# Kernel tuning notes

Measured on AMD Instinct MI355X. Metric: run time of the kernel, lower is better.

## Reference

```python
import jax, jax.numpy as jnp
import numpy as np

N_DST = 50000
NUM_HEAD = 2
LN_EPS = 1e-5


def setup_inputs() -> dict:
    key = jax.random.key(0)
    ks = jax.random.split(key, 12)
    n_dst, n_src, E = 50000, 200000, 250000
    dim_node, dim_edge, dim_time, dim_out = 128, 64, 64, 128
    d_q = dim_node + dim_time            # w_q input dim
    d_k = dim_node + dim_edge + dim_time  # w_k / w_v input dim
    d_o = dim_node + dim_out              # w_out input dim
    f32 = jnp.float32
    return {
        "h": jax.random.normal(ks[0], (n_dst + n_src, dim_node), f32),
        "dt": jax.random.uniform(ks[1], (E,), f32) * 100.0,
        "ef": jax.random.normal(ks[2], (E, dim_edge), f32),
        # TimeEncode: cos(t * w + b), classic TGAT init w = 1/10^linspace(0,9)
        "time_w": (1.0 / 10.0 ** jnp.linspace(0.0, 9.0, dim_time)).astype(f32),
        "time_b": jnp.zeros((dim_time,), f32),
        "wq_w": (jax.random.normal(ks[3], (d_q, dim_out), f32) / np.sqrt(d_q)),
        "wq_b": jnp.zeros((dim_out,), f32),
        "wk_w": (jax.random.normal(ks[4], (d_k, dim_out), f32) / np.sqrt(d_k)),
        "wk_b": jnp.zeros((dim_out,), f32),
        "wv_w": (jax.random.normal(ks[5], (d_k, dim_out), f32) / np.sqrt(d_k)),
        "wv_b": jnp.zeros((dim_out,), f32),
        "wo_w": (jax.random.normal(ks[6], (d_o, dim_out), f32) / np.sqrt(d_o)),
        "wo_b": jnp.zeros((dim_out,), f32),
        "ln_g": jnp.ones((dim_out,), f32),
        "ln_b": jnp.zeros((dim_out,), f32),
        "nbr_idx": jax.random.randint(ks[7], (E,), 0, n_src),
        "edge_dst": jax.random.randint(ks[8], (E,), 0, n_dst),
    }


def reference(h, dt, ef, time_w, time_b, wq_w, wq_b, wk_w, wk_b, wv_w, wv_b,
              wo_w, wo_b, ln_g, ln_b, nbr_idx, edge_dst):
    n_dst = N_DST
    H = NUM_HEAD
    h_dst = h[:n_dst]                       # [n_dst, D]
    h_src = h[n_dst:]                       # [n_src, D]

    # time encoding: cos(t * w + b)
    time_feat = jnp.cos(dt[:, None] * time_w + time_b)          # [E, Dt]
    zero_time = jnp.broadcast_to(jnp.cos(time_b), (n_dst, time_b.shape[0]))

    Q_in = jnp.concatenate([h_dst, zero_time], axis=1)           # [n_dst, D+Dt]
    K_in = jnp.concatenate([h_src[nbr_idx], ef, time_feat], axis=1)  # [E, D+De+Dt]

    Q = (Q_in @ wq_w + wq_b)[edge_dst]      # [E, dim_out] gathered per edge
    K = K_in @ wk_w + wk_b                  # [E, dim_out]
    V = K_in @ wv_w + wv_b                  # [E, dim_out]

    E_ = Q.shape[0]
    Qh = Q.reshape(E_, H, -1)
    Kh = K.reshape(E_, H, -1)
    Vh = V.reshape(E_, H, -1)

    att_raw = jax.nn.leaky_relu(jnp.sum(Qh * Kh, axis=2), 0.2)   # [E, H]

    # edge_softmax: segment softmax over incoming edges of each dst node
    m = jax.ops.segment_max(att_raw, edge_dst, num_segments=n_dst)
    m = jnp.where(jnp.isfinite(m), m, 0.0)  # guard empty segments
    ex = jnp.exp(att_raw - m[edge_dst])
    den = jax.ops.segment_sum(ex, edge_dst, num_segments=n_dst)
    att = ex / den[edge_dst]                # [E, H]

    Vw = (Vh * att[..., None]).reshape(E_, -1)                   # [E, dim_out]
    agg = jax.ops.segment_sum(Vw, edge_dst, num_segments=n_dst)  # [n_dst, dim_out]

    pre = jax.nn.relu(jnp.concatenate([agg, h_dst], axis=1) @ wo_w + wo_b)
    mu = jnp.mean(pre, axis=-1, keepdims=True)
    var = jnp.var(pre, axis=-1, keepdims=True)
    return (pre - mu) / jnp.sqrt(var + LN_EPS) * ln_g + ln_b
```

## Files before the change

### kernel.cpp

```cpp
#include <hip/hip_runtime.h>
#include <hip/hip_bf16.h>
#include <math.h>


using bf16 = __hip_bfloat16;
typedef __attribute__((ext_vector_type(8))) short short8;
typedef __attribute__((ext_vector_type(4))) float f32x4;

static __device__ __forceinline__ unsigned short bf16_bits(float x) {
    bf16 h = __float2bfloat16(x);
    unsigned short b;
    __builtin_memcpy(&b, &h, 2);
    return b;
}
static __device__ __forceinline__ unsigned pk2(float x, float y) {
    return (unsigned)bf16_bits(x) | ((unsigned)bf16_bits(y) << 16);
}
static __device__ __forceinline__ float bflo(unsigned u) {
    return __uint_as_float(u << 16);
}
static __device__ __forceinline__ float bfhi(unsigned u) {
    return __uint_as_float(u & 0xffff0000u);
}
union frag_u { short8 s; unsigned u[4]; };

__global__ void k_prep(float* qbias, const float* __restrict__ wq_w,
                       const float* __restrict__ wq_b, const float* __restrict__ time_b) {
    int c = threadIdx.x;
    if (c < 128) {
        float s = wq_b[c];
        for (int j = 0; j < 64; ++j)
            s += cosf(time_b[j]) * wq_w[(128 + j) * 128 + c];
        qbias[c] = s;
    }
}

__global__ void k_pack(unsigned short* wkT, unsigned short* wvT, unsigned short* woT,
                       unsigned short* wqhT, unsigned short* wqlT,
                       const float* __restrict__ wk_w, const float* __restrict__ wv_w,
                       const float* __restrict__ wo_w, const float* __restrict__ wq_w) {
    int idx = blockIdx.x * blockDim.x + threadIdx.x;
    if (idx < 32768) {
        int n = idx >> 8, k = idx & 255;
        wkT[idx] = bf16_bits(wk_w[(size_t)k * 128 + n]);
        wvT[idx] = bf16_bits(wv_w[(size_t)k * 128 + n]);
        woT[idx] = bf16_bits(wo_w[(size_t)k * 128 + n]);
        if (idx < 16384) {
            int n2 = idx >> 7, k2 = idx & 127;
            float v = wq_w[(size_t)k2 * 128 + n2];
            unsigned short hb = bf16_bits(v);
            wqhT[idx] = hb;
            wqlT[idx] = bf16_bits(v - __uint_as_float((unsigned)hb << 16));
        }
    }
}

__global__ void k_count(const int* __restrict__ edst, int* cnt, int E) {
    int e = blockIdx.x * 256 + threadIdx.x;
    if (e < E) atomicAdd(&cnt[edst[e]], 1);
}

__global__ void k_scan1(const int* __restrict__ cnt, int* rs, int* bsum, int n) {
    __shared__ int s[256];
    int t = threadIdx.x;
    int i = blockIdx.x * 256 + t;
    int v = (i < n) ? cnt[i] : 0;
    s[t] = v;
    __syncthreads();
    for (int off = 1; off < 256; off <<= 1) {
        int x = (t >= off) ? s[t - off] : 0;
        __syncthreads();
        s[t] += x;
        __syncthreads();
    }
    if (i < n) rs[i] = s[t] - v;
    if (t == 255) bsum[blockIdx.x] = s[255];
}

__global__ void k_scan2(int* bsum, int nblk) {
    __shared__ int s[256];
    int t = threadIdx.x;
    int v = (t < nblk) ? bsum[t] : 0;
    s[t] = v;
    __syncthreads();
    for (int off = 1; off < 256; off <<= 1) {
        int x = (t >= off) ? s[t - off] : 0;
        __syncthreads();
        s[t] += x;
        __syncthreads();
    }
    if (t < nblk) bsum[t] = s[t] - v;
}

__global__ void k_scan3(int* rs, const int* __restrict__ bsum, int n) {
    int i = blockIdx.x * 256 + threadIdx.x;
    if (i < n) rs[i] += bsum[blockIdx.x];
}

__global__ void k_scatter(const int* __restrict__ edst, const int* __restrict__ rs,
                          int* fill, int* epos, int E) {
    int e = blockIdx.x * 256 + threadIdx.x;
    if (e < E) {
        int d = edst[e];
        epos[e] = rs[d] + atomicAdd(&fill[d], 1);
    }
}

__global__ __launch_bounds__(256) void k_q(
    float* __restrict__ Q, const float* __restrict__ h,
    const unsigned short* __restrict__ wqhT, const unsigned short* __restrict__ wqlT,
    const float* __restrict__ qbias, int ndst)
{
    __shared__ unsigned short Bs[16384];
    int tid = threadIdx.x;
    int lane = tid & 63, l15 = lane & 15, lk = lane >> 4;
    int r0 = blockIdx.x * 64 + (tid >> 6) * 16;
    int ra = r0 + l15;
    int rc = (ra < ndst) ? ra : (ndst - 1);
    const float* hrow = h + (size_t)rc * 128;

    float4 hx[4][2];
    #pragma unroll
    for (int kk = 0; kk < 4; ++kk) {
        int c0 = kk * 32 + lk * 8;
        hx[kk][0] = *reinterpret_cast<const float4*>(hrow + c0);
        hx[kk][1] = *reinterpret_cast<const float4*>(hrow + c0 + 4);
    }

    #pragma unroll
    for (int it = 0; it < 8; ++it) {
        int i = it * 256 + tid;
        int row = i >> 4, c = i & 15;
        uint4 v = *reinterpret_cast<const uint4*>(wqhT + (size_t)row * 128 + c * 8);
        *reinterpret_cast<uint4*>(Bs + row * 128 + ((c ^ (row & 15)) << 3)) = v;
    }

    frag_u ah[4], al[4];
    #pragma unroll
    for (int kk = 0; kk < 4; ++kk) {
        float xs[8] = {hx[kk][0].x, hx[kk][0].y, hx[kk][0].z, hx[kk][0].w,
                       hx[kk][1].x, hx[kk][1].y, hx[kk][1].z, hx[kk][1].w};
        unsigned short hb[8];
        float lo[8];
        #pragma unroll
        for (int t = 0; t < 8; ++t) {
            hb[t] = bf16_bits(xs[t]);
            lo[t] = xs[t] - __uint_as_float((unsigned)hb[t] << 16);
        }
        #pragma unroll
        for (int t = 0; t < 4; ++t)
            ah[kk].u[t] = (unsigned)hb[2*t] | ((unsigned)hb[2*t+1] << 16);
        al[kk].u[0] = pk2(lo[0], lo[1]); al[kk].u[1] = pk2(lo[2], lo[3]);
        al[kk].u[2] = pk2(lo[4], lo[5]); al[kk].u[3] = pk2(lo[6], lo[7]);
    }

    f32x4 ck[8];
    #pragma unroll
    for (int nt = 0; nt < 8; ++nt) ck[nt] = (f32x4){0.f, 0.f, 0.f, 0.f};

    __syncthreads();
    #pragma unroll
    for (int kk2 = 0; kk2 < 4; ++kk2) {
        int co = ((kk2 * 4 + lk) ^ l15) << 3;
        #pragma unroll
        for (int nt = 0; nt < 8; ++nt) {
            short8 b = *reinterpret_cast<const short8*>(Bs + (nt * 16 + l15) * 128 + co);
            ck[nt] = __builtin_amdgcn_mfma_f32_16x16x32_bf16(ah[kk2].s, b, ck[nt], 0, 0, 0);
            ck[nt] = __builtin_amdgcn_mfma_f32_16x16x32_bf16(al[kk2].s, b, ck[nt], 0, 0, 0);
        }
    }
    __syncthreads();
    #pragma unroll
    for (int it = 0; it < 8; ++it) {
        int i = it * 256 + tid;
        int row = i >> 4, c = i & 15;
        uint4 v = *reinterpret_cast<const uint4*>(wqlT + (size_t)row * 128 + c * 8);
        *reinterpret_cast<uint4*>(Bs + row * 128 + ((c ^ (row & 15)) << 3)) = v;
    }
    __syncthreads();
    #pragma unroll
    for (int kk2 = 0; kk2 < 4; ++kk2) {
        int co = ((kk2 * 4 + lk) ^ l15) << 3;
        #pragma unroll
        for (int nt = 0; nt < 8; ++nt) {
            short8 b = *reinterpret_cast<const short8*>(Bs + (nt * 16 + l15) * 128 + co);
            ck[nt] = __builtin_amdgcn_mfma_f32_16x16x32_bf16(ah[kk2].s, b, ck[nt], 0, 0, 0);
        }
    }

    #pragma unroll
    for (int nt = 0; nt < 8; ++nt) {
        int col = nt * 16 + l15;
        float qb = qbias[col];
        #pragma unroll
        for (int j = 0; j < 4; ++j) {
            int row = r0 + lk * 4 + j;
            if (row < ndst) Q[(size_t)row * 128 + col] = ck[nt][j] + qb;
        }
    }
}

__global__ __launch_bounds__(256) void k_kvA(
    const float* __restrict__ h, const int* __restrict__ nbr, const int* __restrict__ edst,
    const float* __restrict__ dt, const float* __restrict__ ef,
    const float* __restrict__ time_w, const float* __restrict__ time_b,
    const unsigned short* __restrict__ wkT, const unsigned short* __restrict__ wvT,
    const float* __restrict__ wk_b, const float* __restrict__ Q,
    const int* __restrict__ epos,
    unsigned short* __restrict__ Vbuf, float2* __restrict__ att2, int ndst, int E)
{
    __shared__ unsigned short Bs[16384];
    int tid  = threadIdx.x;
    int lane = tid & 63;
    int l15  = lane & 15;
    int lk   = lane >> 4;
    int e0   = blockIdx.x * 64 + (tid >> 6) * 16;

    int  ea = e0 + l15;
    bool va = ea < E;
    int  na = va ? nbr[ea] : 0;
    float da = va ? dt[ea] : 0.f;
    const float* hrow = h + (size_t)(ndst + na) * 128;
    const float* erow = ef + (size_t)ea * 64;

    int dstr[4], pe[4];
    bool evv[4];
    #pragma unroll
    for (int j = 0; j < 4; ++j) {
        int ed = e0 + lk * 4 + j;
        evv[j]  = ed < E;
        dstr[j] = evv[j] ? edst[ed] : 0;
        pe[j]   = evv[j] ? epos[ed] : 0;
    }

    float4 hx[4][2], ex_[2][2];
    const float4 z4 = make_float4(0.f, 0.f, 0.f, 0.f);
    #pragma unroll
    for (int kk = 0; kk < 4; ++kk) {
        int c0 = kk * 32 + lk * 8;
        hx[kk][0] = va ? *reinterpret_cast<const float4*>(hrow + c0)     : z4;
        hx[kk][1] = va ? *reinterpret_cast<const float4*>(hrow + c0 + 4) : z4;
    }
    #pragma unroll
    for (int t = 0; t < 2; ++t) {
        int c = (4 + t) * 32 + lk * 8 - 128;
        ex_[t][0] = va ? *reinterpret_cast<const float4*>(erow + c)     : z4;
        ex_[t][1] = va ? *reinterpret_cast<const float4*>(erow + c + 4) : z4;
    }

    float qg[8][4];
    #pragma unroll
    for (int nt = 0; nt < 8; ++nt) {
        int gc = nt * 16 + l15;
        #pragma unroll
        for (int j = 0; j < 4; ++j)
            qg[nt][j] = Q[(size_t)dstr[j] * 128 + gc];
    }

    #pragma unroll
    for (int it = 0; it < 8; ++it) {
        int i = it * 256 + tid;
        int row = i >> 4, c = i & 15;
        uint4 v = *reinterpret_cast<const uint4*>(wkT + (size_t)row * 256 + c * 8);
        *reinterpret_cast<uint4*>(Bs + row * 128 + ((c ^ (row & 15)) << 3)) = v;
    }

    float tf[16];
    {
        int j0 = lk * 8;
        #pragma unroll
        for (int t = 0; t < 8; ++t) tf[t]     = __cosf(fmaf(da, time_w[j0 + t],      time_b[j0 + t]));
        #pragma unroll
        for (int t = 0; t < 8; ++t) tf[8 + t] = __cosf(fmaf(da, time_w[j0 + 32 + t], time_b[j0 + 32 + t]));
    }

    frag_u a[8];
    #pragma unroll
    for (int kk = 0; kk < 4; ++kk) {
        a[kk].u[0] = pk2(hx[kk][0].x, hx[kk][0].y); a[kk].u[1] = pk2(hx[kk][0].z, hx[kk][0].w);
        a[kk].u[2] = pk2(hx[kk][1].x, hx[kk][1].y); a[kk].u[3] = pk2(hx[kk][1].z, hx[kk][1].w);
    }
    #pragma unroll
    for (int t = 0; t < 2; ++t) {
        a[4+t].u[0] = pk2(ex_[t][0].x, ex_[t][0].y); a[4+t].u[1] = pk2(ex_[t][0].z, ex_[t][0].w);
        a[4+t].u[2] = pk2(ex_[t][1].x, ex_[t][1].y); a[4+t].u[3] = pk2(ex_[t][1].z, ex_[t][1].w);
    }
    a[6].u[0] = pk2(tf[0], tf[1]);  a[6].u[1] = pk2(tf[2], tf[3]);
    a[6].u[2] = pk2(tf[4], tf[5]);  a[6].u[3] = pk2(tf[6], tf[7]);
    a[7].u[0] = pk2(tf[8], tf[9]);  a[7].u[1] = pk2(tf[10], tf[11]);
    a[7].u[2] = pk2(tf[12], tf[13]); a[7].u[3] = pk2(tf[14], tf[15]);

    f32x4 ck[8];
    #pragma unroll
    for (int nt = 0; nt < 8; ++nt) ck[nt] = (f32x4){0.f, 0.f, 0.f, 0.f};

    __syncthreads();
    #pragma unroll
    for (int kk2 = 0; kk2 < 4; ++kk2) {
        int co = ((kk2 * 4 + lk) ^ l15) << 3;
        #pragma unroll
        for (int nt = 0; nt < 8; ++nt) {
            short8 b = *reinterpret_cast<const short8*>(Bs + (nt * 16 + l15) * 128 + co);
            ck[nt] = __builtin_amdgcn_mfma_f32_16x16x32_bf16(a[kk2].s, b, ck[nt], 0, 0, 0);
        }
    }
    __syncthreads();
    #pragma unroll
    for (int it = 0; it < 8; ++it) {
        int i = it * 256 + tid;
        int row = i >> 4, c = i & 15;
        uint4 v = *reinterpret_cast<const uint4*>(wkT + (size_t)row * 256 + 128 + c * 8);
        *reinterpret_cast<uint4*>(Bs + row * 128 + ((c ^ (row & 15)) << 3)) = v;
    }
    __syncthreads();
    #pragma unroll
    for (int kk2 = 0; kk2 < 4; ++kk2) {
        int co = ((kk2 * 4 + lk) ^ l15) << 3;
        #pragma unroll
        for (int nt = 0; nt < 8; ++nt) {
            short8 b = *reinterpret_cast<const short8*>(Bs + (nt * 16 + l15) * 128 + co);
            ck[nt] = __builtin_amdgcn_mfma_f32_16x16x32_bf16(a[4 + kk2].s, b, ck[nt], 0, 0, 0);
        }
    }
    __syncthreads();
    #pragma unroll
    for (int it = 0; it < 8; ++it) {
        int i = it * 256 + tid;
        int row = i >> 4, c = i & 15;
        uint4 v = *reinterpret_cast<const uint4*>(wvT + (size_t)row * 256 + c * 8);
        *reinterpret_cast<uint4*>(Bs + row * 128 + ((c ^ (row & 15)) << 3)) = v;
    }

    float p0[4], p1[4];
    #pragma unroll
    for (int j = 0; j < 4; ++j) { p0[j] = 0.f; p1[j] = 0.f; }
    #pragma unroll
    for (int nt = 0; nt < 8; ++nt) {
        float kb = wk_b[nt * 16 + l15];
        #pragma unroll
        for (int j = 0; j < 4; ++j) {
            float t = (ck[nt][j] + kb) * qg[nt][j];
            if (nt < 4) p0[j] += t; else p1[j] += t;
        }
    }
    #pragma unroll
    for (int m = 1; m <= 8; m <<= 1)
        #pragma unroll
        for (int j = 0; j < 4; ++j) {
            p0[j] += __shfl_xor(p0[j], m, 64);
            p1[j] += __shfl_xor(p1[j], m, 64);
        }
    if (l15 == 0) {
        #pragma unroll
        for (int j = 0; j < 4; ++j)
            if (evv[j]) {
                float r0 = p0[j]; r0 = (r0 >= 0.f) ? r0 : 0.2f * r0;
                float r1 = p1[j]; r1 = (r1 >= 0.f) ? r1 : 0.2f * r1;
                att2[pe[j]] = make_float2(r0, r1);
            }
    }

    f32x4 cv[8];
    #pragma unroll
    for (int nt = 0; nt < 8; ++nt) cv[nt] = (f32x4){0.f, 0.f, 0.f, 0.f};
    __syncthreads();
    #pragma unroll
    for (int kk2 = 0; kk2 < 4; ++kk2) {
        int co = ((kk2 * 4 + lk) ^ l15) << 3;
        #pragma unroll
        for (int nt = 0; nt < 8; ++nt) {
            short8 b = *reinterpret_cast<const short8*>(Bs + (nt * 16 + l15) * 128 + co);
            cv[nt] = __builtin_amdgcn_mfma_f32_16x16x32_bf16(a[kk2].s, b, cv[nt], 0, 0, 0);
        }
    }
    __syncthreads();
    #pragma unroll
    for (int it = 0; it < 8; ++it) {
        int i = it * 256 + tid;
        int row = i >> 4, c = i & 15;
        uint4 v = *reinterpret_cast<const uint4*>(wvT + (size_t)row * 256 + 128 + c * 8);
        *reinterpret_cast<uint4*>(Bs + row * 128 + ((c ^ (row & 15)) << 3)) = v;
    }
    __syncthreads();
    #pragma unroll
    for (int kk2 = 0; kk2 < 4; ++kk2) {
        int co = ((kk2 * 4 + lk) ^ l15) << 3;
        #pragma unroll
        for (int nt = 0; nt < 8; ++nt) {
            short8 b = *reinterpret_cast<const short8*>(Bs + (nt * 16 + l15) * 128 + co);
            cv[nt] = __builtin_amdgcn_mfma_f32_16x16x32_bf16(a[4 + kk2].s, b, cv[nt], 0, 0, 0);
        }
    }

    #pragma unroll
    for (int j = 0; j < 4; ++j)
        if (evv[j]) {
            uint4 val;
            val.x = pk2(cv[0][j], cv[1][j]);
            val.y = pk2(cv[2][j], cv[3][j]);
            val.z = pk2(cv[4][j], cv[5][j]);
            val.w = pk2(cv[6][j], cv[7][j]);
            *reinterpret_cast<uint4*>(Vbuf + (size_t)pe[j] * 128 + l15 * 8) = val;
        }
}

__global__ __launch_bounds__(256) void k_agg(
    const unsigned short* __restrict__ Vbuf, const float2* __restrict__ att2,
    const int* __restrict__ rs, const int* __restrict__ cnt,
    const float* __restrict__ wv_b, float* __restrict__ agg, int ndst)
{
    int w = threadIdx.x >> 6, lane = threadIdx.x & 63;
    int d = blockIdx.x * 4 + w;
    if (d >= ndst) return;
    int p0 = lane * 2, p1 = p0 + 1;
    int c0 = ((p0 & 7) << 4) + (p0 >> 3);
    int c1 = ((p1 & 7) << 4) + (p1 >> 3);
    bool h0 = (p0 & 4) != 0, h1 = (p1 & 4) != 0;
    int base = rs[d], n = cnt[d];
    const unsigned* V32 = reinterpret_cast<const unsigned*>(Vbuf);
    float den0 = 0.f, den1 = 0.f, acc0 = 0.f, acc1 = 0.f;
    for (int i = 0; i < n; ++i) {
        size_t row = (size_t)(base + i);
        float2 at = att2[row];
        float ex0 = __expf(at.x), ex1 = __expf(at.y);
        den0 += ex0; den1 += ex1;
        unsigned vv = V32[row * 64 + lane];
        acc0 = fmaf(h0 ? ex1 : ex0, bflo(vv), acc0);
        acc1 = fmaf(h1 ? ex1 : ex0, bfhi(vv), acc1);
    }
    float o0 = 0.f, o1 = 0.f;
    if (n > 0) {
        o0 = acc0 / (h0 ? den1 : den0) + wv_b[c0];
        o1 = acc1 / (h1 ? den1 : den0) + wv_b[c1];
    }
    agg[(size_t)d * 128 + c0] = o0;
    agg[(size_t)d * 128 + c1] = o1;
}

__global__ __launch_bounds__(256) void k_out(
    const float* __restrict__ agg, const float* __restrict__ h,
    const unsigned short* __restrict__ woT, const float* __restrict__ wo_b,
    const float* __restrict__ ln_g, const float* __restrict__ ln_b,
    float* __restrict__ out, int ndst)
{
    __shared__ unsigned short Bs[16384];
    int tid = threadIdx.x;
    int lane = tid & 63, l15 = lane & 15, lk = lane >> 4;
    int r0 = blockIdx.x * 64 + (tid >> 6) * 16;
    int ra = r0 + l15;
    int rc = (ra < ndst) ? ra : (ndst - 1);
    const float* arow = agg + (size_t)rc * 128;
    const float* hrow = h + (size_t)rc * 128;

    float4 ax[4][2], hx[4][2];
    #pragma unroll
    for (int kk = 0; kk < 4; ++kk) {
        int c0 = kk * 32 + lk * 8;
        ax[kk][0] = *reinterpret_cast<const float4*>(arow + c0);
        ax[kk][1] = *reinterpret_cast<const float4*>(arow + c0 + 4);
        hx[kk][0] = *reinterpret_cast<const float4*>(hrow + c0);
        hx[kk][1] = *reinterpret_cast<const float4*>(hrow + c0 + 4);
    }

    #pragma unroll
    for (int it = 0; it < 8; ++it) {
        int i = it * 256 + tid;
        int row = i >> 4, c = i & 15;
        uint4 v = *reinterpret_cast<const uint4*>(woT + (size_t)row * 256 + c * 8);
        *reinterpret_cast<uint4*>(Bs + row * 128 + ((c ^ (row & 15)) << 3)) = v;
    }

    frag_u aa[4], ah[4];
    #pragma unroll
    for (int kk = 0; kk < 4; ++kk) {
        aa[kk].u[0] = pk2(ax[kk][0].x, ax[kk][0].y); aa[kk].u[1] = pk2(ax[kk][0].z, ax[kk][0].w);
        aa[kk].u[2] = pk2(ax[kk][1].x, ax[kk][1].y); aa[kk].u[3] = pk2(ax[kk][1].z, ax[kk][1].w);
        ah[kk].u[0] = pk2(hx[kk][0].x, hx[kk][0].y); ah[kk].u[1] = pk2(hx[kk][0].z, hx[kk][0].w);
        ah[kk].u[2] = pk2(hx[kk][1].x, hx[kk][1].y); ah[kk].u[3] = pk2(hx[kk][1].z, hx[kk][1].w);
    }

    f32x4 ck[8];
    #pragma unroll
    for (int nt = 0; nt < 8; ++nt) ck[nt] = (f32x4){0.f, 0.f, 0.f, 0.f};

    __syncthreads();
    #pragma unroll
    for (int kk2 = 0; kk2 < 4; ++kk2) {
        int co = ((kk2 * 4 + lk) ^ l15) << 3;
        #pragma unroll
        for (int nt = 0; nt < 8; ++nt) {
            short8 b = *reinterpret_cast<const short8*>(Bs + (nt * 16 + l15) * 128 + co);
            ck[nt] = __builtin_amdgcn_mfma_f32_16x16x32_bf16(aa[kk2].s, b, ck[nt], 0, 0, 0);
        }
    }
    __syncthreads();
    #pragma unroll
    for (int it = 0; it < 8; ++it) {
        int i = it * 256 + tid;
        int row = i >> 4, c = i & 15;
        uint4 v = *reinterpret_cast<const uint4*>(woT + (size_t)row * 256 + 128 + c * 8);
        *reinterpret_cast<uint4*>(Bs + row * 128 + ((c ^ (row & 15)) << 3)) = v;
    }
    __syncthreads();
    #pragma unroll
    for (int kk2 = 0; kk2 < 4; ++kk2) {
        int co = ((kk2 * 4 + lk) ^ l15) << 3;
        #pragma unroll
        for (int nt = 0; nt < 8; ++nt) {
            short8 b = *reinterpret_cast<const short8*>(Bs + (nt * 16 + l15) * 128 + co);
            ck[nt] = __builtin_amdgcn_mfma_f32_16x16x32_bf16(ah[kk2].s, b, ck[nt], 0, 0, 0);
        }
    }

    #pragma unroll
    for (int nt = 0; nt < 8; ++nt) {
        float bo = wo_b[nt * 16 + l15];
        #pragma unroll
        for (int j = 0; j < 4; ++j)
            ck[nt][j] = fmaxf(ck[nt][j] + bo, 0.f);
    }
    float s1[4], s2[4];
    #pragma unroll
    for (int j = 0; j < 4; ++j) { s1[j] = 0.f; s2[j] = 0.f; }
    #pragma unroll
    for (int nt = 0; nt < 8; ++nt)
        #pragma unroll
        for (int j = 0; j < 4; ++j) {
            s1[j] += ck[nt][j];
            s2[j] = fmaf(ck[nt][j], ck[nt][j], s2[j]);
        }
    #pragma unroll
    for (int m = 1; m <= 8; m <<= 1)
        #pragma unroll
        for (int j = 0; j < 4; ++j) {
            s1[j] += __shfl_xor(s1[j], m, 64);
            s2[j] += __shfl_xor(s2[j], m, 64);
        }
    float mean[4], rstd[4];
    #pragma unroll
    for (int j = 0; j < 4; ++j) {
        mean[j] = s1[j] * (1.f / 128.f);
        float var = s2[j] * (1.f / 128.f) - mean[j] * mean[j];
        rstd[j] = rsqrtf(var + 1e-5f);
    }
    #pragma unroll
    for (int nt = 0; nt < 8; ++nt) {
        int col = nt * 16 + l15;
        float g = ln_g[col], lb = ln_b[col];
        #pragma unroll
        for (int j = 0; j < 4; ++j) {
            int row = r0 + lk * 4 + j;
            if (row < ndst)
                out[(size_t)row * 128 + col] = (ck[nt][j] - mean[j]) * rstd[j] * g + lb;
        }
    }
}

extern "C" void kernel_launch(void* const* d_in, const int* in_sizes, int n_in,
                              void* d_out, int out_size, void* d_ws, size_t ws_size,
                              hipStream_t stream) {
    const float* h      = (const float*)d_in[0];
    const float* dt     = (const float*)d_in[1];
    const float* ef     = (const float*)d_in[2];
    const float* time_w = (const float*)d_in[3];
    const float* time_b = (const float*)d_in[4];
    const float* wq_w   = (const float*)d_in[5];
    const float* wq_b   = (const float*)d_in[6];
    const float* wk_w   = (const float*)d_in[7];
    const float* wk_b   = (const float*)d_in[8];
    const float* wv_w   = (const float*)d_in[9];
    const float* wv_b   = (const float*)d_in[10];
    const float* wo_w   = (const float*)d_in[11];
    const float* wo_b   = (const float*)d_in[12];
    const float* ln_g   = (const float*)d_in[13];
    const float* ln_b   = (const float*)d_in[14];
    const int* nbr      = (const int*)d_in[15];
    const int* edst     = (const int*)d_in[16];

    int E    = in_sizes[1];
    int ndst = out_size / 128;
    int nblk = (ndst + 255) / 256;

    char* wsb = (char*)d_ws;
    float* qbias = (float*)wsb;                 wsb += 512;
    float* Q     = (float*)wsb;                 wsb += (size_t)ndst * 128 * 4;
    float* agg   = (float*)wsb;                 wsb += (size_t)ndst * 128 * 4;
    unsigned short* wkT  = (unsigned short*)wsb; wsb += 32768 * 2;
    unsigned short* wvT  = (unsigned short*)wsb; wsb += 32768 * 2;
    unsigned short* woT  = (unsigned short*)wsb; wsb += 32768 * 2;
    unsigned short* wqhT = (unsigned short*)wsb; wsb += 16384 * 2;
    unsigned short* wqlT = (unsigned short*)wsb; wsb += 16384 * 2;
    int* cnt    = (int*)wsb;                    wsb += (size_t)ndst * 4;
    int* fill   = (int*)wsb;                    wsb += (size_t)ndst * 4;
    int* rs     = (int*)wsb;                    wsb += (size_t)ndst * 4;
    int* bsum   = (int*)wsb;                    wsb += 1024;
    int* epos   = (int*)wsb;                    wsb += (size_t)E * 4;
    float2* att2 = (float2*)wsb;                wsb += (size_t)E * 8;
    unsigned short* Vbuf = (unsigned short*)wsb; wsb += (size_t)E * 128 * 2;

    hipMemsetAsync(cnt, 0, (size_t)ndst * 8, stream);
    k_prep<<<1, 128, 0, stream>>>(qbias, wq_w, wq_b, time_b);
    k_pack<<<128, 256, 0, stream>>>(wkT, wvT, woT, wqhT, wqlT, wk_w, wv_w, wo_w, wq_w);
    k_count<<<(E + 255) / 256, 256, 0, stream>>>(edst, cnt, E);
    k_scan1<<<nblk, 256, 0, stream>>>(cnt, rs, bsum, ndst);
    k_scan2<<<1, 256, 0, stream>>>(bsum, nblk);
    k_scan3<<<nblk, 256, 0, stream>>>(rs, bsum, ndst);
    k_scatter<<<(E + 255) / 256, 256, 0, stream>>>(edst, rs, fill, epos, E);
    k_q<<<(ndst + 63) / 64, 256, 0, stream>>>(Q, h, wqhT, wqlT, qbias, ndst);
    k_kvA<<<(E + 63) / 64, 256, 0, stream>>>(h, nbr, edst, dt, ef, time_w, time_b,
                                             wkT, wvT, wk_b, Q, epos, Vbuf, att2, ndst, E);
    k_agg<<<(ndst + 3) / 4, 256, 0, stream>>>(Vbuf, att2, rs, cnt, wv_b, agg, ndst);
    k_out<<<(ndst + 63) / 64, 256, 0, stream>>>(agg, h, woT, wo_b, ln_g, ln_b,
                                                (float*)d_out, ndst);
}
```

Before: 248.9 us.

## Stage full weight matrices in shared memory, widen blocks, merge small kernels

Doubles the shared-memory tile so the GEMM kernels (Q, K/V, output) hold the full K=256 weight matrix, or both the hi and lo halves for Q, at once. This removes the mid-kernel reload and the extra barriers, and blocks grow to 512 threads covering 128 rows. The qbias prep is folded into the pack kernel, and the scan3 pass is dropped by adding the block offset at use sites. The aggregation loop is unrolled by four to overlap loads. The larger shared-memory footprint per block may reduce occupancy.

```diff
diff --git a/kernel.cpp b/kernel.cpp
--- a/kernel.cpp
+++ b/kernel.cpp
@@ -24,21 +24,11 @@
 }
 union frag_u { short8 s; unsigned u[4]; };
 
-__global__ void k_prep(float* qbias, const float* __restrict__ wq_w,
+__global__ void k_pack(unsigned short* wkT, unsigned short* wvT, unsigned short* woT,
+                       unsigned short* wqhT, unsigned short* wqlT, float* qbias,
+                       const float* __restrict__ wk_w, const float* __restrict__ wv_w,
+                       const float* __restrict__ wo_w, const float* __restrict__ wq_w,
                        const float* __restrict__ wq_b, const float* __restrict__ time_b) {
-    int c = threadIdx.x;
-    if (c < 128) {
-        float s = wq_b[c];
-        for (int j = 0; j < 64; ++j)
-            s += cosf(time_b[j]) * wq_w[(128 + j) * 128 + c];
-        qbias[c] = s;
-    }
-}
-
-__global__ void k_pack(unsigned short* wkT, unsigned short* wvT, unsigned short* woT,
-                       unsigned short* wqhT, unsigned short* wqlT,
-                       const float* __restrict__ wk_w, const float* __restrict__ wv_w,
-                       const float* __restrict__ wo_w, const float* __restrict__ wq_w) {
     int idx = blockIdx.x * blockDim.x + threadIdx.x;
     if (idx < 32768) {
         int n = idx >> 8, k = idx & 255;
@@ -52,6 +42,12 @@
             wqhT[idx] = hb;
             wqlT[idx] = bf16_bits(v - __uint_as_float((unsigned)hb << 16));
         }
+        if (idx < 128) {
+            float s = wq_b[idx];
+            for (int j = 0; j < 64; ++j)
+                s += cosf(time_b[j]) * wq_w[(128 + j) * 128 + idx];
+            qbias[idx] = s;
+        }
     }
 }
 
@@ -92,29 +88,24 @@
     if (t < nblk) bsum[t] = s[t] - v;
 }
 
-__global__ void k_scan3(int* rs, const int* __restrict__ bsum, int n) {
-    int i = blockIdx.x * 256 + threadIdx.x;
-    if (i < n) rs[i] += bsum[blockIdx.x];
-}
-
 __global__ void k_scatter(const int* __restrict__ edst, const int* __restrict__ rs,
-                          int* fill, int* epos, int E) {
+                          const int* __restrict__ bsum, int* fill, int* epos, int E) {
     int e = blockIdx.x * 256 + threadIdx.x;
     if (e < E) {
         int d = edst[e];
-        epos[e] = rs[d] + atomicAdd(&fill[d], 1);
-    }
-}
-
-__global__ __launch_bounds__(256) void k_q(
+        epos[e] = rs[d] + bsum[d >> 8] + atomicAdd(&fill[d], 1);
+    }
+}
+
+__global__ __launch_bounds__(512) void k_q(
     float* __restrict__ Q, const float* __restrict__ h,
     const unsigned short* __restrict__ wqhT, const unsigned short* __restrict__ wqlT,
     const float* __restrict__ qbias, int ndst)
 {
-    __shared__ unsigned short Bs[16384];
+    __shared__ unsigned short Bs[32768];
     int tid = threadIdx.x;
     int lane = tid & 63, l15 = lane & 15, lk = lane >> 4;
-    int r0 = blockIdx.x * 64 + (tid >> 6) * 16;
+    int r0 = blockIdx.x * 128 + (tid >> 6) * 16;
     int ra = r0 + l15;
     int rc = (ra < ndst) ? ra : (ndst - 1);
     const float* hrow = h + (size_t)rc * 128;
@@ -128,11 +119,14 @@
     }
 
     #pragma unroll
-    for (int it = 0; it < 8; ++it) {
-        int i = it * 256 + tid;
+    for (int it = 0; it < 4; ++it) {
+        int i = it * 512 + tid;
         int row = i >> 4, c = i & 15;
+        int sw = ((c ^ (row & 15)) << 3);
         uint4 v = *reinterpret_cast<const uint4*>(wqhT + (size_t)row * 128 + c * 8);
-        *reinterpret_cast<uint4*>(Bs + row * 128 + ((c ^ (row & 15)) << 3)) = v;
+        *reinterpret_cast<uint4*>(Bs + row * 128 + sw) = v;
+        uint4 w = *reinterpret_cast<const uint4*>(wqlT + (size_t)row * 128 + c * 8);
+        *reinterpret_cast<uint4*>(Bs + 16384 + row * 128 + sw) = w;
     }
 
     frag_u ah[4], al[4];
@@ -164,27 +158,12 @@
         int co = ((kk2 * 4 + lk) ^ l15) << 3;
         #pragma unroll
         for (int nt = 0; nt < 8; ++nt) {
-            short8 b = *reinterpret_cast<const short8*>(Bs + (nt * 16 + l15) * 128 + co);
-            ck[nt] = __builtin_amdgcn_mfma_f32_16x16x32_bf16(ah[kk2].s, b, ck[nt], 0, 0, 0);
-            ck[nt] = __builtin_amdgcn_mfma_f32_16x16x32_bf16(al[kk2].s, b, ck[nt], 0, 0, 0);
-        }
-    }
-    __syncthreads();
-    #pragma unroll
-    for (int it = 0; it < 8; ++it) {
-        int i = it * 256 + tid;
-        int row = i >> 4, c = i & 15;
-        uint4 v = *reinterpret_cast<const uint4*>(wqlT + (size_t)row * 128 + c * 8);
-        *reinterpret_cast<uint4*>(Bs + row * 128 + ((c ^ (row & 15)) << 3)) = v;
-    }
-    __syncthreads();
-    #pragma unroll
-    for (int kk2 = 0; kk2 < 4; ++kk2) {
-        int co = ((kk2 * 4 + lk) ^ l15) << 3;
-        #pragma unroll
-        for (int nt = 0; nt < 8; ++nt) {
-            short8 b = *reinterpret_cast<const short8*>(Bs + (nt * 16 + l15) * 128 + co);
-            ck[nt] = __builtin_amdgcn_mfma_f32_16x16x32_bf16(ah[kk2].s, b, ck[nt], 0, 0, 0);
+            int ro = (nt * 16 + l15) * 128;
+            short8 bh = *reinterpret_cast<const short8*>(Bs + ro + co);
+            short8 bl = *reinterpret_cast<const short8*>(Bs + 16384 + ro + co);
+            ck[nt] = __builtin_amdgcn_mfma_f32_16x16x32_bf16(ah[kk2].s, bh, ck[nt], 0, 0, 0);
+            ck[nt] = __builtin_amdgcn_mfma_f32_16x16x32_bf16(al[kk2].s, bh, ck[nt], 0, 0, 0);
+            ck[nt] = __builtin_amdgcn_mfma_f32_16x16x32_bf16(ah[kk2].s, bl, ck[nt], 0, 0, 0);
         }
     }
 
@@ -200,7 +179,7 @@
     }
 }
 
-__global__ __launch_bounds__(256) void k_kvA(
+__global__ __launch_bounds__(512) void k_kvA(
     const float* __restrict__ h, const int* __restrict__ nbr, const int* __restrict__ edst,
     const float* __restrict__ dt, const float* __restrict__ ef,
     const float* __restrict__ time_w, const float* __restrict__ time_b,
@@ -209,12 +188,12 @@
     const int* __restrict__ epos,
     unsigned short* __restrict__ Vbuf, float2* __restrict__ att2, int ndst, int E)
 {
-    __shared__ unsigned short Bs[16384];
+    __shared__ unsigned short Bs[32768];
     int tid  = threadIdx.x;
     int lane = tid & 63;
     int l15  = lane & 15;
     int lk   = lane >> 4;
-    int e0   = blockIdx.x * 64 + (tid >> 6) * 16;
+    int e0   = blockIdx.x * 128 + (tid >> 6) * 16;
 
     int  ea = e0 + l15;
     bool va = ea < E;
@@ -259,10 +238,10 @@
 
     #pragma unroll
     for (int it = 0; it < 8; ++it) {
-        int i = it * 256 + tid;
-        int row = i >> 4, c = i & 15;
+        int i = it * 512 + tid;
+        int row = i >> 5, c = i & 31;
         uint4 v = *reinterpret_cast<const uint4*>(wkT + (size_t)row * 256 + c * 8);
-        *reinterpret_cast<uint4*>(Bs + row * 128 + ((c ^ (row & 15)) << 3)) = v;
+        *reinterpret_cast<uint4*>(Bs + row * 256 + ((c ^ (row & 15)) << 3)) = v;
     }
 
     float tf[16];
@@ -296,39 +275,21 @@
 
     __syncthreads();
     #pragma unroll
-    for (int kk2 = 0; kk2 < 4; ++kk2) {
+    for (int kk2 = 0; kk2 < 8; ++kk2) {
         int co = ((kk2 * 4 + lk) ^ l15) << 3;
         #pragma unroll
         for (int nt = 0; nt < 8; ++nt) {
-            short8 b = *reinterpret_cast<const short8*>(Bs + (nt * 16 + l15) * 128 + co);
+            short8 b = *reinterpret_cast<const short8*>(Bs + (nt * 16 + l15) * 256 + co);
             ck[nt] = __builtin_amdgcn_mfma_f32_16x16x32_bf16(a[kk2].s, b, ck[nt], 0, 0, 0);
         }
     }
     __syncthreads();
     #pragma unroll
     for (int it = 0; it < 8; ++it) {
-        int i = it * 256 + tid;
-        int row = i >> 4, c = i & 15;
-        uint4 v = *reinterpret_cast<const uint4*>(wkT + (size_t)row * 256 + 128 + c * 8);
-        *reinterpret_cast<uint4*>(Bs + row * 128 + ((c ^ (row & 15)) << 3)) = v;
-    }
-    __syncthreads();
-    #pragma unroll
-    for (int kk2 = 0; kk2 < 4; ++kk2) {
-        int co = ((kk2 * 4 + lk) ^ l15) << 3;
-        #pragma unroll
-        for (int nt = 0; nt < 8; ++nt) {
-            short8 b = *reinterpret_cast<const short8*>(Bs + (nt * 16 + l15) * 128 + co);
-            ck[nt] = __builtin_amdgcn_mfma_f32_16x16x32_bf16(a[4 + kk2].s, b, ck[nt], 0, 0, 0);
-        }
-    }
-    __syncthreads();
-    #pragma unroll
-    for (int it = 0; it < 8; ++it) {
-        int i = it * 256 + tid;
-        int row = i >> 4, c = i & 15;
+        int i = it * 512 + tid;
+        int row = i >> 5, c = i & 31;
         uint4 v = *reinterpret_cast<const uint4*>(wvT + (size_t)row * 256 + c * 8);
-        *reinterpret_cast<uint4*>(Bs + row * 128 + ((c ^ (row & 15)) << 3)) = v;
+        *reinterpret_cast<uint4*>(Bs + row * 256 + ((c ^ (row & 15)) << 3)) = v;
     }
 
     float p0[4], p1[4];
@@ -365,30 +326,12 @@
     for (int nt = 0; nt < 8; ++nt) cv[nt] = (f32x4){0.f, 0.f, 0.f, 0.f};
     __syncthreads();
     #pragma unroll
-    for (int kk2 = 0; kk2 < 4; ++kk2) {
+    for (int kk2 = 0; kk2 < 8; ++kk2) {
         int co = ((kk2 * 4 + lk) ^ l15) << 3;
         #pragma unroll
         for (int nt = 0; nt < 8; ++nt) {
-            short8 b = *reinterpret_cast<const short8*>(Bs + (nt * 16 + l15) * 128 + co);
+            short8 b = *reinterpret_cast<const short8*>(Bs + (nt * 16 + l15) * 256 + co);
             cv[nt] = __builtin_amdgcn_mfma_f32_16x16x32_bf16(a[kk2].s, b, cv[nt], 0, 0, 0);
-        }
-    }
-    __syncthreads();
-    #pragma unroll
-    for (int it = 0; it < 8; ++it) {
-        int i = it * 256 + tid;
-        int row = i >> 4, c = i & 15;
-        uint4 v = *reinterpret_cast<const uint4*>(wvT + (size_t)row * 256 + 128 + c * 8);
-        *reinterpret_cast<uint4*>(Bs + row * 128 + ((c ^ (row & 15)) << 3)) = v;
-    }
-    __syncthreads();
-    #pragma unroll
-    for (int kk2 = 0; kk2 < 4; ++kk2) {
-        int co = ((kk2 * 4 + lk) ^ l15) << 3;
-        #pragma unroll
-        for (int nt = 0; nt < 8; ++nt) {
-            short8 b = *reinterpret_cast<const short8*>(Bs + (nt * 16 + l15) * 128 + co);
-            cv[nt] = __builtin_amdgcn_mfma_f32_16x16x32_bf16(a[4 + kk2].s, b, cv[nt], 0, 0, 0);
         }
     }
 
@@ -406,7 +349,7 @@
 
 __global__ __launch_bounds__(256) void k_agg(
     const unsigned short* __restrict__ Vbuf, const float2* __restrict__ att2,
-    const int* __restrict__ rs, const int* __restrict__ cnt,
+    const int* __restrict__ rs, const int* __restrict__ bsum, const int* __restrict__ cnt,
     const float* __restrict__ wv_b, float* __restrict__ agg, int ndst)
 {
     int w = threadIdx.x >> 6, lane = threadIdx.x & 63;
@@ -416,15 +359,36 @@
     int c0 = ((p0 & 7) << 4) + (p0 >> 3);
     int c1 = ((p1 & 7) << 4) + (p1 >> 3);
     bool h0 = (p0 & 4) != 0, h1 = (p1 & 4) != 0;
-    int base = rs[d], n = cnt[d];
+    int base = rs[d] + bsum[d >> 8], n = cnt[d];
     const unsigned* V32 = reinterpret_cast<const unsigned*>(Vbuf);
     float den0 = 0.f, den1 = 0.f, acc0 = 0.f, acc1 = 0.f;
-    for (int i = 0; i < n; ++i) {
-        size_t row = (size_t)(base + i);
-        float2 at = att2[row];
+    int i = 0;
+    for (; i + 4 <= n; i += 4) {
+        size_t r = (size_t)(base + i);
+        float2 a0 = att2[r], a1 = att2[r+1], a2 = att2[r+2], a3 = att2[r+3];
+        unsigned w0 = V32[r*64 + lane], w1 = V32[(r+1)*64 + lane];
+        unsigned w2 = V32[(r+2)*64 + lane], w3 = V32[(r+3)*64 + lane];
+        float e00 = __expf(a0.x), e01 = __expf(a0.y);
+        float e10 = __expf(a1.x), e11 = __expf(a1.y);
+        float e20 = __expf(a2.x), e21 = __expf(a2.y);
+        float e30 = __expf(a3.x), e31 = __expf(a3.y);
+        den0 += e00 + e10 + e20 + e30;
+        den1 += e01 + e11 + e21 + e31;
+        acc0 = fmaf(h0 ? e01 : e00, bflo(w0), acc0);
+        acc1 = fmaf(h1 ? e01 : e00, bfhi(w0), acc1);
+        acc0 = fmaf(h0 ? e11 : e10, bflo(w1), acc0);
+        acc1 = fmaf(h1 ? e11 : e10, bfhi(w1), acc1);
+        acc0 = fmaf(h0 ? e21 : e20, bflo(w2), acc0);
+        acc1 = fmaf(h1 ? e21 : e20, bfhi(w2), acc1);
+        acc0 = fmaf(h0 ? e31 : e30, bflo(w3), acc0);
+        acc1 = fmaf(h1 ? e31 : e30, bfhi(w3), acc1);
+    }
+    for (; i < n; ++i) {
+        size_t r = (size_t)(base + i);
+        float2 at = att2[r];
         float ex0 = __expf(at.x), ex1 = __expf(at.y);
         den0 += ex0; den1 += ex1;
-        unsigned vv = V32[row * 64 + lane];
+        unsigned vv = V32[r*64 + lane];
         acc0 = fmaf(h0 ? ex1 : ex0, bflo(vv), acc0);
         acc1 = fmaf(h1 ? ex1 : ex0, bfhi(vv), acc1);
     }
@@ -437,16 +401,16 @@
     agg[(size_t)d * 128 + c1] = o1;
 }
 
-__global__ __launch_bounds__(256) void k_out(
+__global__ __launch_bounds__(512) void k_out(
     const float* __restrict__ agg, const float* __restrict__ h,
     const unsigned short* __restrict__ woT, const float* __restrict__ wo_b,
     const float* __restrict__ ln_g, const float* __restrict__ ln_b,
     float* __restrict__ out, int ndst)
 {
-    __shared__ unsigned short Bs[16384];
+    __shared__ unsigned short Bs[32768];
     int tid = threadIdx.x;
     int lane = tid & 63, l15 = lane & 15, lk = lane >> 4;
-    int r0 = blockIdx.x * 64 + (tid >> 6) * 16;
+    int r0 = blockIdx.x * 128 + (tid >> 6) * 16;
     int ra = r0 + l15;
     int rc = (ra < ndst) ? ra : (ndst - 1);
     const float* arow = agg + (size_t)rc * 128;
@@ -464,10 +428,10 @@
 
     #pragma unroll
     for (int it = 0; it < 8; ++it) {
-        int i = it * 256 + tid;
-        int row = i >> 4, c = i & 15;
+        int i = it * 512 + tid;
+        int row = i >> 5, c = i & 31;
         uint4 v = *reinterpret_cast<const uint4*>(woT + (size_t)row * 256 + c * 8);
-        *reinterpret_cast<uint4*>(Bs + row * 128 + ((c ^ (row & 15)) << 3)) = v;
+        *reinterpret_cast<uint4*>(Bs + row * 256 + ((c ^ (row & 15)) << 3)) = v;
     }
 
     frag_u aa[4], ah[4];
@@ -486,29 +450,15 @@
     __syncthreads();
     #pragma unroll
     for (int kk2 = 0; kk2 < 4; ++kk2) {
-        int co = ((kk2 * 4 + lk) ^ l15) << 3;
+        int coA = ((kk2 * 4 + lk) ^ l15) << 3;
+        int coH = (((16 + kk2 * 4 + lk)) ^ l15) << 3;
         #pragma unroll
         for (int nt = 0; nt < 8; ++nt) {
-            short8 b = *reinterpret_cast<const short8*>(Bs + (nt * 16 + l15) * 128 + co);
-            ck[nt] = __builtin_amdgcn_mfma_f32_16x16x32_bf16(aa[kk2].s, b, ck[nt], 0, 0, 0);
-        }
-    }
-    __syncthreads();
-    #pragma unroll
-    for (int it = 0; it < 8; ++it) {
-        int i = it * 256 + tid;
-        int row = i >> 4, c = i & 15;
-        uint4 v = *reinterpret_cast<const uint4*>(woT + (size_t)row * 256 + 128 + c * 8);
-        *reinterpret_cast<uint4*>(Bs + row * 128 + ((c ^ (row & 15)) << 3)) = v;
-    }
-    __syncthreads();
-    #pragma unroll
-    for (int kk2 = 0; kk2 < 4; ++kk2) {
-        int co = ((kk2 * 4 + lk) ^ l15) << 3;
-        #pragma unroll
-        for (int nt = 0; nt < 8; ++nt) {
-            short8 b = *reinterpret_cast<const short8*>(Bs + (nt * 16 + l15) * 128 + co);
-            ck[nt] = __builtin_amdgcn_mfma_f32_16x16x32_bf16(ah[kk2].s, b, ck[nt], 0, 0, 0);
+            int ro = (nt * 16 + l15) * 256;
+            short8 bA = *reinterpret_cast<const short8*>(Bs + ro + coA);
+            short8 bH = *reinterpret_cast<const short8*>(Bs + ro + coH);
+            ck[nt] = __builtin_amdgcn_mfma_f32_16x16x32_bf16(aa[kk2].s, bA, ck[nt], 0, 0, 0);
+            ck[nt] = __builtin_amdgcn_mfma_f32_16x16x32_bf16(ah[kk2].s, bH, ck[nt], 0, 0, 0);
         }
     }
 
@@ -599,17 +549,16 @@
     unsigned short* Vbuf = (unsigned short*)wsb; wsb += (size_t)E * 128 * 2;
 
     hipMemsetAsync(cnt, 0, (size_t)ndst * 8, stream);
-    k_prep<<<1, 128, 0, stream>>>(qbias, wq_w, wq_b, time_b);
-    k_pack<<<128, 256, 0, stream>>>(wkT, wvT, woT, wqhT, wqlT, wk_w, wv_w, wo_w, wq_w);
+    k_pack<<<128, 256, 0, stream>>>(wkT, wvT, woT, wqhT, wqlT, qbias,
+                                    wk_w, wv_w, wo_w, wq_w, wq_b, time_b);
     k_count<<<(E + 255) / 256, 256, 0, stream>>>(edst, cnt, E);
     k_scan1<<<nblk, 256, 0, stream>>>(cnt, rs, bsum, ndst);
     k_scan2<<<1, 256, 0, stream>>>(bsum, nblk);
-    k_scan3<<<nblk, 256, 0, stream>>>(rs, bsum, ndst);
-    k_scatter<<<(E + 255) / 256, 256, 0, stream>>>(edst, rs, fill, epos, E);
-    k_q<<<(ndst + 63) / 64, 256, 0, stream>>>(Q, h, wqhT, wqlT, qbias, ndst);
-    k_kvA<<<(E + 63) / 64, 256, 0, stream>>>(h, nbr, edst, dt, ef, time_w, time_b,
-                                             wkT, wvT, wk_b, Q, epos, Vbuf, att2, ndst, E);
-    k_agg<<<(ndst + 3) / 4, 256, 0, stream>>>(Vbuf, att2, rs, cnt, wv_b, agg, ndst);
-    k_out<<<(ndst + 63) / 64, 256, 0, stream>>>(agg, h, woT, wo_b, ln_g, ln_b,
-                                                (float*)d_out, ndst);
-}
+    k_scatter<<<(E + 255) / 256, 256, 0, stream>>>(edst, rs, bsum, fill, epos, E);
+    k_q<<<(ndst + 127) / 128, 512, 0, stream>>>(Q, h, wqhT, wqlT, qbias, ndst);
+    k_kvA<<<(E + 127) / 128, 512, 0, stream>>>(h, nbr, edst, dt, ef, time_w, time_b,
+                                               wkT, wvT, wk_b, Q, epos, Vbuf, att2, ndst, E);
+    k_agg<<<(ndst + 3) / 4, 256, 0, stream>>>(Vbuf, att2, rs, bsum, cnt, wv_b, agg, ndst);
+    k_out<<<(ndst + 127) / 128, 512, 0, stream>>>(agg, h, woT, wo_b, ln_g, ln_b,
+                                                  (float*)d_out, ndst);
+}
```

New measurement: 247.8 us. About the same (-0.4%).
